# Kernel tuning notes

Measured on AMD Instinct MI355X. Metric: run time of the kernel, lower is better.

Reference implementation:

```python
import jax, jax.numpy as jnp
import numpy as np

TEMP = 0.5
EPS = 1e-8  # torch CosineSimilarity eps


def setup_inputs() -> dict:
    key = jax.random.key(0)
    k1, k2 = jax.random.split(key)
    B, D = 4096, 512
    z_i = jax.random.normal(k1, (B, D), dtype=jnp.float32)
    z_j = jax.random.normal(k2, (B, D), dtype=jnp.float32)
    return {"z_i": z_i, "z_j": z_j}


def reference(z_i, z_j):
    B = z_i.shape[0]
    N = 2 * B
    z = jnp.concatenate([z_i, z_j], axis=0)              # [N, D]
    norm = jnp.maximum(jnp.linalg.norm(z, axis=1, keepdims=True), EPS)
    zn = z / norm                                        # unit rows
    sim = jnp.matmul(zn, zn.T) / TEMP                    # [N, N] cosine sims / temperature
    # positives: sim[i, i+B] for i<B and sim[i+B, i] for i<B
    pos = jnp.concatenate([jnp.diagonal(sim, offset=B), jnp.diagonal(sim, offset=-B)])  # [N]
    # CE over logits [pos, negatives] with label 0 == -pos + logsumexp(row without diagonal)
    diag_mask = jnp.eye(N, dtype=bool)
    sim_masked = jnp.where(diag_mask, -jnp.inf, sim)
    lse = jax.nn.logsumexp(sim_masked, axis=1)           # [N]
    loss = jnp.sum(lse - pos) / N                        # CrossEntropyLoss(reduction='sum') / N
    return loss
```

## Files before the change

### kernel.cpp

```cpp
#include <hip/hip_runtime.h>
#include <stdint.h>

#define NROWS 8192
#define HALF_N 4096
#define DIM 512
#define INV_TEMP 2.0f
#define E2SCALE 2.8853900817779268f
#define LN2 0.6931471805599453f
#define NTILES 2080

typedef int i32x8 __attribute__((ext_vector_type(8)));
typedef float f32x16 __attribute__((ext_vector_type(16)));

__device__ __forceinline__ void gload_lds16(const unsigned char* g, unsigned char* l) {
  __builtin_amdgcn_global_load_lds(
      (const __attribute__((address_space(1))) unsigned int*)(uintptr_t)g,
      (__attribute__((address_space(3))) unsigned int*)(uint32_t)(uintptr_t)l,
      16, 0, 0);
}

__global__ void __launch_bounds__(256) k_normalize(const float* __restrict__ zi,
                                                   const float* __restrict__ zj,
                                                   unsigned char* __restrict__ zn,
                                                   float* __restrict__ sumexp) {
  int tid = threadIdx.x;
  int gid = blockIdx.x * 256 + tid;
  if (gid < NROWS) sumexp[gid] = 0.0f;
  int wave = tid >> 6, lane = tid & 63;
  int row = blockIdx.x * 4 + wave;
  const float* src = (row < HALF_N) ? (zi + (size_t)row * DIM)
                                    : (zj + (size_t)(row - HALF_N) * DIM);
  const float4* s4 = (const float4*)src;
  float4 a = s4[lane];
  float4 b = s4[lane + 64];
  float ss = a.x * a.x + a.y * a.y + a.z * a.z + a.w * a.w +
             b.x * b.x + b.y * b.y + b.z * b.z + b.w * b.w;
#pragma unroll
  for (int off = 32; off > 0; off >>= 1) ss += __shfl_xor(ss, off, 64);
  float inv = 1.0f / fmaxf(sqrtf(ss), 1e-8f);
  int w0 = __builtin_amdgcn_cvt_pk_fp8_f32(a.x * inv, a.y * inv, 0, false);
  w0 = __builtin_amdgcn_cvt_pk_fp8_f32(a.z * inv, a.w * inv, w0, true);
  int w1 = __builtin_amdgcn_cvt_pk_fp8_f32(b.x * inv, b.y * inv, 0, false);
  w1 = __builtin_amdgcn_cvt_pk_fp8_f32(b.z * inv, b.w * inv, w1, true);
  unsigned char* dst = zn + (size_t)row * DIM;
  *((int*)(dst + lane * 4)) = w0;
  *((int*)(dst + 256 + lane * 4)) = w1;
}

__global__ void __launch_bounds__(256) k_simsum(const unsigned char* __restrict__ zn,
                                                float* __restrict__ sumexp,
                                                float* __restrict__ posv) {
  __shared__ __align__(16) unsigned char As[2][128 * 64];
  __shared__ __align__(16) unsigned char Bs[2][128 * 64];
  int tid = threadIdx.x;
  int wave = tid >> 6, lane = tid & 63;

  int idx = blockIdx.x;
  int tn = (int)((sqrtf(8.0f * idx + 1.0f) - 1.0f) * 0.5f);
  while (tn * (tn + 1) / 2 > idx) tn--;
  while ((tn + 1) * (tn + 2) / 2 <= idx) tn++;
  int tm = idx - tn * (tn + 1) / 2;
  int rowBase = tm * 128, colBase = tn * 128;
  int wr = (wave >> 1) * 64, wc = (wave & 1) * 64;
  int h = lane >> 5, c32 = lane & 31;

  int rA = wave * 32 + (lane >> 2);
  int chunk = (lane & 3) ^ ((rA >> 1) & 3);
  const unsigned char* gA = zn + (size_t)(rowBase + rA) * DIM + chunk * 16;
  const unsigned char* gB = zn + (size_t)(colBase + rA) * DIM + chunk * 16;
  unsigned char* lA[2] = {&As[0][wave * 2048], &As[1][wave * 2048]};
  unsigned char* lB[2] = {&Bs[0][wave * 2048], &Bs[1][wave * 2048]};

#define STAGE(b)                                  \
  do {                                            \
    gload_lds16(gA, lA[b]);                       \
    gload_lds16(gA + 16 * DIM, lA[b] + 1024);     \
    gload_lds16(gB, lB[b]);                       \
    gload_lds16(gB + 16 * DIM, lB[b] + 1024);     \
    gA += 64; gB += 64;                           \
  } while (0)

  f32x16 acc[2][2];
#pragma unroll
  for (int i = 0; i < 2; i++)
#pragma unroll
    for (int j = 0; j < 2; j++)
#pragma unroll
      for (int r = 0; r < 16; r++) acc[i][j][r] = 0.f;

  int sg = (c32 >> 1) & 3;
  int p0 = (2 * h) ^ sg, p1 = p0 ^ 1;
  int aIdx[2] = {(wr + c32) * 4, (wr + 32 + c32) * 4};
  int bIdx[2] = {(wc + c32) * 4, (wc + 32 + c32) * 4};

#define COMPUTE(b)                                                                   \
  do {                                                                               \
    const int4* Av = (const int4*)As[b];                                             \
    const int4* Bv = (const int4*)Bs[b];                                             \
    i32x8 af[2], bfr[2];                                                             \
    _Pragma("unroll") for (int i = 0; i < 2; i++) {                                  \
      int4 lo = Av[aIdx[i] + p0], hi = Av[aIdx[i] + p1];                             \
      af[i] = (i32x8){lo.x, lo.y, lo.z, lo.w, hi.x, hi.y, hi.z, hi.w};               \
    }                                                                                \
    _Pragma("unroll") for (int j = 0; j < 2; j++) {                                  \
      int4 lo = Bv[bIdx[j] + p0], hi = Bv[bIdx[j] + p1];                             \
      bfr[j] = (i32x8){lo.x, lo.y, lo.z, lo.w, hi.x, hi.y, hi.z, hi.w};              \
    }                                                                                \
    _Pragma("unroll") for (int i = 0; i < 2; i++)                                    \
      _Pragma("unroll") for (int j = 0; j < 2; j++)                                  \
        acc[i][j] = __builtin_amdgcn_mfma_scale_f32_32x32x64_f8f6f4(                 \
            af[i], bfr[j], acc[i][j], 0, 0,                               \
            0, 0x7F, 0, 0x7F);                                     \
  } while (0)

  STAGE(0);
#pragma unroll
  for (int s = 0; s < 8; s += 2) {
    __syncthreads();
    if (s + 1 < 8) STAGE(1);
    COMPUTE(0);
    __syncthreads();
    if (s + 2 < 8) STAGE(0);
    COMPUTE(1);
  }

  bool isDiag = (tm == tn);
  bool hasPos = (tn == tm + 32);
  bool diagLane = (wr == wc) && (h == ((c32 >> 2) & 1));
  int rsel = (c32 & 3) | ((c32 >> 3) << 2);

  if (isDiag && diagLane) {
    acc[0][0][rsel] = -1e30f;
    acc[1][1][rsel] = -1e30f;
  }
  if (hasPos && diagLane) {
#pragma unroll
    for (int i = 0; i < 2; i++) {
      float sv = acc[i][i][rsel] * INV_TEMP;
      int gr = rowBase + wr + i * 32 + c32;
      posv[gr] = sv;
      posv[gr + HALF_N] = sv;
    }
  }

  float rp[32], cp[2] = {0.f, 0.f};
#pragma unroll
  for (int i = 0; i < 2; i++)
#pragma unroll
    for (int r = 0; r < 16; r++) {
      float e0 = __builtin_amdgcn_exp2f(acc[i][0][r] * E2SCALE);
      float e1 = __builtin_amdgcn_exp2f(acc[i][1][r] * E2SCALE);
      rp[i * 16 + r] = e0 + e1;
      cp[0] += e0;
      cp[1] += e1;
    }

#pragma unroll
  for (int t = 0; t < 16; t++) {
    float mine = (lane & 16) ? rp[t + 16] : rp[t];
    float oth = __shfl_xor((lane & 16) ? rp[t] : rp[t + 16], 16, 64);
    rp[t] = mine + oth;
  }
#pragma unroll
  for (int t = 0; t < 8; t++) {
    float mine = (lane & 8) ? rp[t + 8] : rp[t];
    float oth = __shfl_xor((lane & 8) ? rp[t] : rp[t + 8], 8, 64);
    rp[t] = mine + oth;
  }
#pragma unroll
  for (int t = 0; t < 4; t++) {
    float mine = (lane & 4) ? rp[t + 4] : rp[t];
    float oth = __shfl_xor((lane & 4) ? rp[t] : rp[t + 4], 4, 64);
    rp[t] = mine + oth;
  }
#pragma unroll
  for (int t = 0; t < 2; t++) {
    float mine = (lane & 2) ? rp[t + 2] : rp[t];
    float oth = __shfl_xor((lane & 2) ? rp[t] : rp[t + 2], 2, 64);
    rp[t] = mine + oth;
  }
  {
    float mine = (lane & 1) ? rp[1] : rp[0];
    float oth = __shfl_xor((lane & 1) ? rp[0] : rp[1], 1, 64);
    rp[0] = mine + oth;
  }
  int myrow = rowBase + wr + 32 * (c32 >> 4) + (c32 & 3) + 8 * ((c32 >> 2) & 3) + 4 * h;
  atomicAdd(&sumexp[myrow], rp[0]);

  if (!isDiag) {
    cp[0] += __shfl_xor(cp[0], 32, 64);
    cp[1] += __shfl_xor(cp[1], 32, 64);
    float cv = h ? cp[1] : cp[0];
    atomicAdd(&sumexp[colBase + wc + h * 32 + c32], cv);
  }
#undef STAGE
#undef COMPUTE
}

__global__ void __launch_bounds__(1024) k_final(const float* __restrict__ sumexp,
                                                const float* __restrict__ posv,
                                                float* __restrict__ out) {
  __shared__ float red[16];
  int tid = threadIdx.x;
  const float4* se4 = (const float4*)sumexp;
  const float4* pv4 = (const float4*)posv;
  float p = 0.f;
#pragma unroll
  for (int c = 0; c < 2; c++) {
    float4 se = se4[tid * 2 + c];
    float4 pv = pv4[tid * 2 + c];
    p += (__builtin_amdgcn_logf(se.x) + __builtin_amdgcn_logf(se.y) +
          __builtin_amdgcn_logf(se.z) + __builtin_amdgcn_logf(se.w)) * LN2 -
         (pv.x + pv.y + pv.z + pv.w);
  }
#pragma unroll
  for (int off = 32; off > 0; off >>= 1) p += __shfl_xor(p, off, 64);
  int wv = tid >> 6, ln = tid & 63;
  if (ln == 0) red[wv] = p;
  __syncthreads();
  if (tid == 0) {
    float t = 0.f;
    for (int w = 0; w < 16; w++) t += red[w];
    out[0] = t / (float)NROWS;
  }
}

extern "C" void kernel_launch(void* const* d_in, const int* in_sizes, int n_in,
                              void* d_out, int out_size, void* d_ws, size_t ws_size,
                              hipStream_t stream) {
  const float* zi = (const float*)d_in[0];
  const float* zj = (const float*)d_in[1];
  unsigned char* zn = (unsigned char*)d_ws;
  float* sumexp = (float*)((char*)d_ws + (size_t)NROWS * DIM);
  float* posv = sumexp + NROWS;
  float* out = (float*)d_out;

  hipLaunchKernelGGL(k_normalize, dim3(2048), dim3(256), 0, stream, zi, zj, zn, sumexp);
  hipLaunchKernelGGL(k_simsum, dim3(NTILES), dim3(256), 0, stream, zn, sumexp, posv);
  hipLaunchKernelGGL(k_final, dim3(1), dim3(1024), 0, stream, sumexp, posv, out);
}
```

Before: 97.50 us.

## Fuse final reduction into simsum via last-block ticket and swizzle tiles per XCD

Removes the separate single-block k_final launch: each simsum block takes an atomic ticket after its atomics, and the last block computes the log-sum and loss. It also remaps block indices so consecutive tiles land on the same XCD for L2 reuse, adds a launch-bounds occupancy hint, and reuses acc registers for the row partials instead of a separate rp array to cut register pressure. The risks are the memory ordering of relaxed atomics around the ticket and a serialized tail reduction inside the last block.

```diff
diff --git a/kernel.cpp b/kernel.cpp
--- a/kernel.cpp
+++ b/kernel.cpp
@@ -8,6 +8,8 @@
 #define E2SCALE 2.8853900817779268f
 #define LN2 0.6931471805599453f
 #define NTILES 2080
+#define NXCD 8
+#define TPX (NTILES / NXCD)
 
 typedef int i32x8 __attribute__((ext_vector_type(8)));
 typedef float f32x16 __attribute__((ext_vector_type(16)));
@@ -22,10 +24,12 @@
 __global__ void __launch_bounds__(256) k_normalize(const float* __restrict__ zi,
                                                    const float* __restrict__ zj,
                                                    unsigned char* __restrict__ zn,
-                                                   float* __restrict__ sumexp) {
+                                                   float* __restrict__ sumexp,
+                                                   unsigned int* __restrict__ ticket) {
   int tid = threadIdx.x;
   int gid = blockIdx.x * 256 + tid;
   if (gid < NROWS) sumexp[gid] = 0.0f;
+  if (gid == 0) *ticket = 0u;
   int wave = tid >> 6, lane = tid & 63;
   int row = blockIdx.x * 4 + wave;
   const float* src = (row < HALF_N) ? (zi + (size_t)row * DIM)
@@ -47,15 +51,20 @@
   *((int*)(dst + 256 + lane * 4)) = w1;
 }
 
-__global__ void __launch_bounds__(256) k_simsum(const unsigned char* __restrict__ zn,
-                                                float* __restrict__ sumexp,
-                                                float* __restrict__ posv) {
+__global__ void __launch_bounds__(256, 4) k_simsum(const unsigned char* __restrict__ zn,
+                                                   float* __restrict__ sumexp,
+                                                   float* __restrict__ posv,
+                                                   unsigned int* __restrict__ ticket,
+                                                   float* __restrict__ out) {
   __shared__ __align__(16) unsigned char As[2][128 * 64];
   __shared__ __align__(16) unsigned char Bs[2][128 * 64];
+  __shared__ unsigned int lastFlag;
+  __shared__ float fred[4];
   int tid = threadIdx.x;
   int wave = tid >> 6, lane = tid & 63;
 
-  int idx = blockIdx.x;
+  int bswz = (blockIdx.x & (NXCD - 1)) * TPX + (blockIdx.x >> 3);
+  int idx = bswz;
   int tn = (int)((sqrtf(8.0f * idx + 1.0f) - 1.0f) * 0.5f);
   while (tn * (tn + 1) / 2 > idx) tn--;
   while ((tn + 1) * (tn + 2) / 2 <= idx) tn++;
@@ -138,54 +147,56 @@
     for (int i = 0; i < 2; i++) {
       float sv = acc[i][i][rsel] * INV_TEMP;
       int gr = rowBase + wr + i * 32 + c32;
-      posv[gr] = sv;
-      posv[gr + HALF_N] = sv;
+      __hip_atomic_store(&posv[gr], sv, __ATOMIC_RELAXED, __HIP_MEMORY_SCOPE_AGENT);
+      __hip_atomic_store(&posv[gr + HALF_N], sv, __ATOMIC_RELAXED, __HIP_MEMORY_SCOPE_AGENT);
     }
   }
 
-  float rp[32], cp[2] = {0.f, 0.f};
+  float cp[2] = {0.f, 0.f};
 #pragma unroll
   for (int i = 0; i < 2; i++)
 #pragma unroll
     for (int r = 0; r < 16; r++) {
       float e0 = __builtin_amdgcn_exp2f(acc[i][0][r] * E2SCALE);
       float e1 = __builtin_amdgcn_exp2f(acc[i][1][r] * E2SCALE);
-      rp[i * 16 + r] = e0 + e1;
       cp[0] += e0;
       cp[1] += e1;
+      acc[i][0][r] = e0 + e1;
     }
 
+#define RP(t) acc[(t) >> 4][0][(t) & 15]
 #pragma unroll
   for (int t = 0; t < 16; t++) {
-    float mine = (lane & 16) ? rp[t + 16] : rp[t];
-    float oth = __shfl_xor((lane & 16) ? rp[t] : rp[t + 16], 16, 64);
-    rp[t] = mine + oth;
+    float mine = (lane & 16) ? RP(t + 16) : RP(t);
+    float oth = __shfl_xor((lane & 16) ? RP(t) : RP(t + 16), 16, 64);
+    RP(t) = mine + oth;
   }
 #pragma unroll
   for (int t = 0; t < 8; t++) {
-    float mine = (lane & 8) ? rp[t + 8] : rp[t];
-    float oth = __shfl_xor((lane & 8) ? rp[t] : rp[t + 8], 8, 64);
-    rp[t] = mine + oth;
+    float mine = (lane & 8) ? RP(t + 8) : RP(t);
+    float oth = __shfl_xor((lane & 8) ? RP(t) : RP(t + 8), 8, 64);
+    RP(t) = mine + oth;
   }
 #pragma unroll
   for (int t = 0; t < 4; t++) {
-    float mine = (lane & 4) ? rp[t + 4] : rp[t];
-    float oth = __shfl_xor((lane & 4) ? rp[t] : rp[t + 4], 4, 64);
-    rp[t] = mine + oth;
+    float mine = (lane & 4) ? RP(t + 4) : RP(t);
+    float oth = __shfl_xor((lane & 4) ? RP(t) : RP(t + 4), 4, 64);
+    RP(t) = mine + oth;
   }
 #pragma unroll
   for (int t = 0; t < 2; t++) {
-    float mine = (lane & 2) ? rp[t + 2] : rp[t];
-    float oth = __shfl_xor((lane & 2) ? rp[t] : rp[t + 2], 2, 64);
-    rp[t] = mine + oth;
+    float mine = (lane & 2) ? RP(t + 2) : RP(t);
+    float oth = __shfl_xor((lane & 2) ? RP(t) : RP(t + 2), 2, 64);
+    RP(t) = mine + oth;
   }
   {
-    float mine = (lane & 1) ? rp[1] : rp[0];
-    float oth = __shfl_xor((lane & 1) ? rp[0] : rp[1], 1, 64);
-    rp[0] = mine + oth;
+    float mine = (lane & 1) ? RP(1) : RP(0);
+    float oth = __shfl_xor((lane & 1) ? RP(0) : RP(1), 1, 64);
+    RP(0) = mine + oth;
   }
   int myrow = rowBase + wr + 32 * (c32 >> 4) + (c32 & 3) + 8 * ((c32 >> 2) & 3) + 4 * h;
-  atomicAdd(&sumexp[myrow], rp[0]);
+  atomicAdd(&sumexp[myrow], RP(0));
+#undef RP
 
   if (!isDiag) {
     cp[0] += __shfl_xor(cp[0], 32, 64);
@@ -193,36 +204,40 @@
     float cv = h ? cp[1] : cp[0];
     atomicAdd(&sumexp[colBase + wc + h * 32 + c32], cv);
   }
+
+  __syncthreads();
+  if (tid == 0) {
+    unsigned int old = __hip_atomic_fetch_add(ticket, 1u, __ATOMIC_RELAXED,
+                                              __HIP_MEMORY_SCOPE_AGENT);
+    lastFlag = (old == (unsigned int)(NTILES - 1)) ? 1u : 0u;
+  }
+  __syncthreads();
+  if (lastFlag) {
+    float p = 0.f;
+#pragma unroll
+    for (int it = 0; it < 8; it++) {
+      int j = it * 1024 + tid;
+      float s0 = __hip_atomic_load(&sumexp[j], __ATOMIC_RELAXED, __HIP_MEMORY_SCOPE_AGENT);
+      float s1 = __hip_atomic_load(&sumexp[j + 256], __ATOMIC_RELAXED, __HIP_MEMORY_SCOPE_AGENT);
+      float s2 = __hip_atomic_load(&sumexp[j + 512], __ATOMIC_RELAXED, __HIP_MEMORY_SCOPE_AGENT);
+      float s3 = __hip_atomic_load(&sumexp[j + 768], __ATOMIC_RELAXED, __HIP_MEMORY_SCOPE_AGENT);
+      float q0 = __hip_atomic_load(&posv[j], __ATOMIC_RELAXED, __HIP_MEMORY_SCOPE_AGENT);
+      float q1 = __hip_atomic_load(&posv[j + 256], __ATOMIC_RELAXED, __HIP_MEMORY_SCOPE_AGENT);
+      float q2 = __hip_atomic_load(&posv[j + 512], __ATOMIC_RELAXED, __HIP_MEMORY_SCOPE_AGENT);
+      float q3 = __hip_atomic_load(&posv[j + 768], __ATOMIC_RELAXED, __HIP_MEMORY_SCOPE_AGENT);
+      p += (__builtin_amdgcn_logf(s0) + __builtin_amdgcn_logf(s1) +
+            __builtin_amdgcn_logf(s2) + __builtin_amdgcn_logf(s3)) * LN2 -
+           (q0 + q1 + q2 + q3);
+    }
+#pragma unroll
+    for (int off = 32; off > 0; off >>= 1) p += __shfl_xor(p, off, 64);
+    if (lane == 0) fred[wave] = p;
+    __syncthreads();
+    if (tid == 0)
+      out[0] = (fred[0] + fred[1] + fred[2] + fred[3]) / (float)NROWS;
+  }
 #undef STAGE
 #undef COMPUTE
-}
-
-__global__ void __launch_bounds__(1024) k_final(const float* __restrict__ sumexp,
-                                                const float* __restrict__ posv,
-                                                float* __restrict__ out) {
-  __shared__ float red[16];
-  int tid = threadIdx.x;
-  const float4* se4 = (const float4*)sumexp;
-  const float4* pv4 = (const float4*)posv;
-  float p = 0.f;
-#pragma unroll
-  for (int c = 0; c < 2; c++) {
-    float4 se = se4[tid * 2 + c];
-    float4 pv = pv4[tid * 2 + c];
-    p += (__builtin_amdgcn_logf(se.x) + __builtin_amdgcn_logf(se.y) +
-          __builtin_amdgcn_logf(se.z) + __builtin_amdgcn_logf(se.w)) * LN2 -
-         (pv.x + pv.y + pv.z + pv.w);
-  }
-#pragma unroll
-  for (int off = 32; off > 0; off >>= 1) p += __shfl_xor(p, off, 64);
-  int wv = tid >> 6, ln = tid & 63;
-  if (ln == 0) red[wv] = p;
-  __syncthreads();
-  if (tid == 0) {
-    float t = 0.f;
-    for (int w = 0; w < 16; w++) t += red[w];
-    out[0] = t / (float)NROWS;
-  }
 }
 
 extern "C" void kernel_launch(void* const* d_in, const int* in_sizes, int n_in,
@@ -233,9 +248,9 @@
   unsigned char* zn = (unsigned char*)d_ws;
   float* sumexp = (float*)((char*)d_ws + (size_t)NROWS * DIM);
   float* posv = sumexp + NROWS;
+  unsigned int* ticket = (unsigned int*)(posv + NROWS);
   float* out = (float*)d_out;
 
-  hipLaunchKernelGGL(k_normalize, dim3(2048), dim3(256), 0, stream, zi, zj, zn, sumexp);
-  hipLaunchKernelGGL(k_simsum, dim3(NTILES), dim3(256), 0, stream, zn, sumexp, posv);
-  hipLaunchKernelGGL(k_final, dim3(1), dim3(1024), 0, stream, sumexp, posv, out);
-}
+  hipLaunchKernelGGL(k_normalize, dim3(2048), dim3(256), 0, stream, zi, zj, zn, sumexp, ticket);
+  hipLaunchKernelGGL(k_simsum, dim3(NTILES), dim3(256), 0, stream, zn, sumexp, posv, ticket, out);
+}
```

Result: slower. 109.0 us (+11.8%).

## Triple-buffer LDS pipeline with vmcnt waits, XCD tile swizzle, and MFMA priority

Applied to the files above, without the earlier changes.

Replaces the double-buffered K loop with a three-stage LDS ring. Each step uses an explicit vmcnt wait and a single barrier, so global-to-LDS loads for step s+2 overlap with compute on step s. Tile indices are remapped so consecutive blocks on the same XCD handle contiguous tiles, which should improve L2 reuse. The MFMA section is raised with s_setprio, and the row-partial array reuses the accumulator registers so the kernel can fit 3 blocks per CU, at the cost of more LDS per block and hand-written waitcnt logic.

```diff
diff --git a/kernel.cpp b/kernel.cpp
--- a/kernel.cpp
+++ b/kernel.cpp
@@ -8,6 +8,8 @@
 #define E2SCALE 2.8853900817779268f
 #define LN2 0.6931471805599453f
 #define NTILES 2080
+#define NXCD 8
+#define TPX (NTILES / NXCD)
 
 typedef int i32x8 __attribute__((ext_vector_type(8)));
 typedef float f32x16 __attribute__((ext_vector_type(16)));
@@ -47,15 +49,16 @@
   *((int*)(dst + 256 + lane * 4)) = w1;
 }
 
-__global__ void __launch_bounds__(256) k_simsum(const unsigned char* __restrict__ zn,
-                                                float* __restrict__ sumexp,
-                                                float* __restrict__ posv) {
-  __shared__ __align__(16) unsigned char As[2][128 * 64];
-  __shared__ __align__(16) unsigned char Bs[2][128 * 64];
+__global__ void __launch_bounds__(256, 3) k_simsum(const unsigned char* __restrict__ zn,
+                                                   float* __restrict__ sumexp,
+                                                   float* __restrict__ posv) {
+  __shared__ __align__(16) unsigned char As[3][128 * 64];
+  __shared__ __align__(16) unsigned char Bs[3][128 * 64];
   int tid = threadIdx.x;
   int wave = tid >> 6, lane = tid & 63;
 
-  int idx = blockIdx.x;
+  int bswz = (blockIdx.x & (NXCD - 1)) * TPX + (blockIdx.x >> 3);
+  int idx = bswz;
   int tn = (int)((sqrtf(8.0f * idx + 1.0f) - 1.0f) * 0.5f);
   while (tn * (tn + 1) / 2 > idx) tn--;
   while ((tn + 1) * (tn + 2) / 2 <= idx) tn++;
@@ -68,16 +71,14 @@
   int chunk = (lane & 3) ^ ((rA >> 1) & 3);
   const unsigned char* gA = zn + (size_t)(rowBase + rA) * DIM + chunk * 16;
   const unsigned char* gB = zn + (size_t)(colBase + rA) * DIM + chunk * 16;
-  unsigned char* lA[2] = {&As[0][wave * 2048], &As[1][wave * 2048]};
-  unsigned char* lB[2] = {&Bs[0][wave * 2048], &Bs[1][wave * 2048]};
-
-#define STAGE(b)                                  \
-  do {                                            \
-    gload_lds16(gA, lA[b]);                       \
-    gload_lds16(gA + 16 * DIM, lA[b] + 1024);     \
-    gload_lds16(gB, lB[b]);                       \
-    gload_lds16(gB + 16 * DIM, lB[b] + 1024);     \
-    gA += 64; gB += 64;                           \
+
+#define STAGE(b)                                          \
+  do {                                                    \
+    gload_lds16(gA, &As[b][wave * 2048]);                 \
+    gload_lds16(gA + 16 * DIM, &As[b][wave * 2048 + 1024]); \
+    gload_lds16(gB, &Bs[b][wave * 2048]);                 \
+    gload_lds16(gB + 16 * DIM, &Bs[b][wave * 2048 + 1024]); \
+    gA += 64; gB += 64;                                   \
   } while (0)
 
   f32x16 acc[2][2];
@@ -106,23 +107,37 @@
       int4 lo = Bv[bIdx[j] + p0], hi = Bv[bIdx[j] + p1];                             \
       bfr[j] = (i32x8){lo.x, lo.y, lo.z, lo.w, hi.x, hi.y, hi.z, hi.w};              \
     }                                                                                \
+    __builtin_amdgcn_s_setprio(1);                                                   \
     _Pragma("unroll") for (int i = 0; i < 2; i++)                                    \
       _Pragma("unroll") for (int j = 0; j < 2; j++)                                  \
         acc[i][j] = __builtin_amdgcn_mfma_scale_f32_32x32x64_f8f6f4(                 \
             af[i], bfr[j], acc[i][j], 0, 0,                               \
             0, 0x7F, 0, 0x7F);                                     \
+    __builtin_amdgcn_s_setprio(0);                                                   \
   } while (0)
 
+#define ASM_VMCNT(n) asm volatile("s_waitcnt vmcnt(" #n ")" ::: "memory")
+#define WINDOW(s, vm)                                        \
+  do {                                                       \
+    ASM_VMCNT(vm);                                           \
+    asm volatile("s_waitcnt lgkmcnt(0)" ::: "memory");       \
+    __builtin_amdgcn_sched_barrier(0);                       \
+    __builtin_amdgcn_s_barrier();                            \
+    __builtin_amdgcn_sched_barrier(0);                       \
+    if ((s) + 2 < 8) STAGE(((s) + 2) % 3);                   \
+    COMPUTE((s) % 3);                                        \
+  } while (0)
+
   STAGE(0);
-#pragma unroll
-  for (int s = 0; s < 8; s += 2) {
-    __syncthreads();
-    if (s + 1 < 8) STAGE(1);
-    COMPUTE(0);
-    __syncthreads();
-    if (s + 2 < 8) STAGE(0);
-    COMPUTE(1);
-  }
+  STAGE(1);
+  WINDOW(0, 4);
+  WINDOW(1, 4);
+  WINDOW(2, 4);
+  WINDOW(3, 4);
+  WINDOW(4, 4);
+  WINDOW(5, 4);
+  WINDOW(6, 4);
+  WINDOW(7, 0);
 
   bool isDiag = (tm == tn);
   bool hasPos = (tn == tm + 32);
@@ -143,49 +158,51 @@
     }
   }
 
-  float rp[32], cp[2] = {0.f, 0.f};
+  float cp[2] = {0.f, 0.f};
 #pragma unroll
   for (int i = 0; i < 2; i++)
 #pragma unroll
     for (int r = 0; r < 16; r++) {
       float e0 = __builtin_amdgcn_exp2f(acc[i][0][r] * E2SCALE);
       float e1 = __builtin_amdgcn_exp2f(acc[i][1][r] * E2SCALE);
-      rp[i * 16 + r] = e0 + e1;
       cp[0] += e0;
       cp[1] += e1;
+      acc[i][0][r] = e0 + e1;
     }
 
+#define RP(t) acc[(t) >> 4][0][(t) & 15]
 #pragma unroll
   for (int t = 0; t < 16; t++) {
-    float mine = (lane & 16) ? rp[t + 16] : rp[t];
-    float oth = __shfl_xor((lane & 16) ? rp[t] : rp[t + 16], 16, 64);
-    rp[t] = mine + oth;
+    float mine = (lane & 16) ? RP(t + 16) : RP(t);
+    float oth = __shfl_xor((lane & 16) ? RP(t) : RP(t + 16), 16, 64);
+    RP(t) = mine + oth;
   }
 #pragma unroll
   for (int t = 0; t < 8; t++) {
-    float mine = (lane & 8) ? rp[t + 8] : rp[t];
-    float oth = __shfl_xor((lane & 8) ? rp[t] : rp[t + 8], 8, 64);
-    rp[t] = mine + oth;
+    float mine = (lane & 8) ? RP(t + 8) : RP(t);
+    float oth = __shfl_xor((lane & 8) ? RP(t) : RP(t + 8), 8, 64);
+    RP(t) = mine + oth;
   }
 #pragma unroll
   for (int t = 0; t < 4; t++) {
-    float mine = (lane & 4) ? rp[t + 4] : rp[t];
-    float oth = __shfl_xor((lane & 4) ? rp[t] : rp[t + 4], 4, 64);
-    rp[t] = mine + oth;
+    float mine = (lane & 4) ? RP(t + 4) : RP(t);
+    float oth = __shfl_xor((lane & 4) ? RP(t) : RP(t + 4), 4, 64);
+    RP(t) = mine + oth;
   }
 #pragma unroll
   for (int t = 0; t < 2; t++) {
-    float mine = (lane & 2) ? rp[t + 2] : rp[t];
-    float oth = __shfl_xor((lane & 2) ? rp[t] : rp[t + 2], 2, 64);
-    rp[t] = mine + oth;
+    float mine = (lane & 2) ? RP(t + 2) : RP(t);
+    float oth = __shfl_xor((lane & 2) ? RP(t) : RP(t + 2), 2, 64);
+    RP(t) = mine + oth;
   }
   {
-    float mine = (lane & 1) ? rp[1] : rp[0];
-    float oth = __shfl_xor((lane & 1) ? rp[0] : rp[1], 1, 64);
-    rp[0] = mine + oth;
+    float mine = (lane & 1) ? RP(1) : RP(0);
+    float oth = __shfl_xor((lane & 1) ? RP(0) : RP(1), 1, 64);
+    RP(0) = mine + oth;
   }
   int myrow = rowBase + wr + 32 * (c32 >> 4) + (c32 & 3) + 8 * ((c32 >> 2) & 3) + 4 * h;
-  atomicAdd(&sumexp[myrow], rp[0]);
+  atomicAdd(&sumexp[myrow], RP(0));
+#undef RP
 
   if (!isDiag) {
     cp[0] += __shfl_xor(cp[0], 32, 64);
@@ -195,6 +212,8 @@
   }
 #undef STAGE
 #undef COMPUTE
+#undef WINDOW
+#undef ASM_VMCNT
 }
 
 __global__ void __launch_bounds__(1024) k_final(const float* __restrict__ sumexp,
```

Measured after the change: 91.73 us (median of 2 runs). 1.06x faster.
